# Performance work log

Measured on AMD Instinct MI355X. Metric: run time of the kernel, lower is better.

## Reference

```python
import jax, jax.numpy as jnp
import numpy as np

B, N, D, V, Y = 4, 4096, 512, 50257, 16000

def setup_inputs() -> dict:
    key = jax.random.key(0)
    ks = jax.random.split(key, 5)
    # token ids in [1, V): avoid pad_id=0 so no attention row is fully -inf
    M_s = jax.random.randint(ks[0], (B, N), 1, V)
    E_v = jax.random.normal(ks[1], (V, D), jnp.float32) * 0.02
    E_y = jax.random.normal(ks[2], (Y, D), jnp.float32) * 0.02
    s = 1.0 / np.sqrt(D)  # kaiming_uniform(a=sqrt(5)) bound for [D,D]
    W_A = jax.random.uniform(ks[3], (D, D), jnp.float32, minval=-s, maxval=s)
    W_O = jax.random.uniform(ks[4], (D, D), jnp.float32, minval=-s, maxval=s)
    gamma = jnp.ones((D,), jnp.float32)
    beta = jnp.zeros((D,), jnp.float32)
    return {"M_s": M_s, "E_v": E_v, "E_y": E_y, "W_A": W_A, "W_O": W_O,
            "gamma": gamma, "beta": beta}

def _layer_norm(x, g, b, eps=1e-5):
    mu = jnp.mean(x, axis=-1, keepdims=True)
    var = jnp.mean(jnp.square(x - mu), axis=-1, keepdims=True)
    return (x - mu) * jax.lax.rsqrt(var + eps) * g + b

def reference(M_s, E_v, E_y, W_A, W_O, gamma, beta):
    # Self-attention branch (v_q=None), dropout in eval mode (identity).
    X = E_v[M_s]                                   # [B, N, D]
    mask = (M_s != 0)                              # [B, N] padding mask
    # logits = (X @ W_A) @ X^T
    logits = jnp.einsum('bnd,de,bme->bnm', X, W_A, X)   # [B, N, N]
    logits = jnp.where(mask[:, None, :], logits, -jnp.inf)
    # positional + causal bias: D = -|i-j| with future (i<j) set to -inf
    i = jnp.arange(N, dtype=jnp.float32)[:, None]
    j = jnp.arange(N, dtype=jnp.float32)[None, :]
    dist = i - j
    bias = jnp.where(dist >= 0, -dist, -jnp.inf)        # [N, N]
    A = jax.nn.softmax(logits + bias, axis=-1)          # [B, N, N]
    Q_c = jnp.einsum('bnm,bmd,de->bne', A, X, W_O)      # [B, N, D]
    H = _layer_norm(Q_c + X, gamma, beta)               # [B, N, D]
    y_logits = jnp.einsum('bnd,yd->bny', H, E_y)        # [B, N, Y]
    return y_logits, A
```

## Files before the change

### kernel.cpp

```cpp
#include <hip/hip_runtime.h>


#define DEVINL __device__ __forceinline__

typedef __attribute__((ext_vector_type(8))) short bf16x8;
typedef __attribute__((ext_vector_type(4))) float f32x4;
typedef unsigned short u16;

#define BB 4
#define NN 4096
#define DD 512
#define YY 16000
#define YPAD 16128
#define ROWS (BB * NN)

DEVINL u16 f2bf(float x) {
  unsigned u = __float_as_uint(x);
  return (u16)((u + 0x7fffu + ((u >> 16) & 1u)) >> 16);
}

DEVINL void gload16(const void* g, void* l) {
  __builtin_amdgcn_global_load_lds(
      (const __attribute__((address_space(1))) void*)g,
      (__attribute__((address_space(3))) void*)l, 16, 0, 0);
}

DEVINL void zero_acc(f32x4 acc[4][4]) {
#pragma unroll
  for (int m = 0; m < 4; ++m)
#pragma unroll
    for (int n = 0; n < 4; ++n) {
      acc[m][n][0] = 0.f; acc[m][n][1] = 0.f;
      acc[m][n][2] = 0.f; acc[m][n][3] = 0.f;
    }
}

DEVINL void gemm_bt_core(const u16* __restrict__ A, int lda,
                         const u16* __restrict__ Bm, int ldb, int ksteps,
                         u16* sA, u16* sB, f32x4 acc[4][4], int tid) {
  const int lane = tid & 63, w = tid >> 6;
  const int wr = (w >> 1) * 64, wc = (w & 1) * 64;
  const int c0 = w * 128 + lane, c1 = c0 + 64;
  const u16* gA0 = A + (size_t)(c0 >> 2) * lda + (c0 & 3) * 8;
  const u16* gA1 = A + (size_t)(c1 >> 2) * lda + (c1 & 3) * 8;
  const u16* gB0 = Bm + (size_t)(c0 >> 2) * ldb + (c0 & 3) * 8;
  const u16* gB1 = Bm + (size_t)(c1 >> 2) * ldb + (c1 & 3) * 8;
  u16* lA0 = sA + w * 1024;  u16* lA1 = lA0 + 512;
  u16* lB0 = sB + w * 1024;  u16* lB1 = lB0 + 512;
  const int fr = lane & 15, fk = (lane >> 4) * 8;

  for (int kt = 0; kt < ksteps; ++kt) {
    __syncthreads();
    gload16(gA0 + kt * 32, lA0);
    gload16(gA1 + kt * 32, lA1);
    gload16(gB0 + kt * 32, lB0);
    gload16(gB1 + kt * 32, lB1);
    __syncthreads();
    bf16x8 af[4], bfv[4];
#pragma unroll
    for (int m = 0; m < 4; ++m)
      af[m] = *(const bf16x8*)(sA + (wr + m * 16 + fr) * 32 + fk);
#pragma unroll
    for (int n = 0; n < 4; ++n)
      bfv[n] = *(const bf16x8*)(sB + (wc + n * 16 + fr) * 32 + fk);
#pragma unroll
    for (int m = 0; m < 4; ++m)
#pragma unroll
      for (int n = 0; n < 4; ++n)
        acc[m][n] = __builtin_amdgcn_mfma_f32_16x16x32_bf16(af[m], bfv[n],
                                                            acc[m][n], 0, 0, 0);
  }
}

__global__ __launch_bounds__(128) void prep_gather(const int* __restrict__ Ms,
                                                   const float* __restrict__ Ev,
                                                   u16* __restrict__ Xb) {
  int row = blockIdx.x, tid = threadIdx.x;
  int tok = Ms[row];
  float4 v = *(const float4*)(Ev + (size_t)tok * DD + tid * 4);
  *(ushort4*)(Xb + (size_t)row * DD + tid * 4) =
      make_ushort4(f2bf(v.x), f2bf(v.y), f2bf(v.z), f2bf(v.w));
}

__global__ __launch_bounds__(256) void prep_wt(const float* __restrict__ W,
                                               u16* __restrict__ Wt) {
  int idx = blockIdx.x * 256 + threadIdx.x;
  int d = idx >> 9, e = idx & 511;
  Wt[(size_t)e * DD + d] = f2bf(W[idx]);
}

__global__ __launch_bounds__(256) void prep_ey(const float* __restrict__ Ey,
                                               u16* __restrict__ Eyb) {
  size_t i4 = (size_t)blockIdx.x * 256 + threadIdx.x;
  size_t row = i4 >> 7;
  ushort4 h;
  if (row < YY) {
    float4 v = *(const float4*)(Ey + i4 * 4);
    h = make_ushort4(f2bf(v.x), f2bf(v.y), f2bf(v.z), f2bf(v.w));
  } else {
    h = make_ushort4(0, 0, 0, 0);
  }
  *(ushort4*)(Eyb + i4 * 4) = h;
}

__global__ __launch_bounds__(256) void prep_xt(const u16* __restrict__ Xb,
                                               u16* __restrict__ XbT) {
  __shared__ u16 t[64][65];
  int tid = threadIdx.x;
  int nt = blockIdx.x, dt = blockIdx.y, b = blockIdx.z;
  const u16* src = Xb + ((size_t)b * NN + nt * 64) * DD + dt * 64;
#pragma unroll
  for (int p = 0; p < 16; ++p) {
    int e = tid + 256 * p; int r = e >> 6, c = e & 63;
    t[r][c] = src[(size_t)r * DD + c];
  }
  __syncthreads();
  u16* dst = XbT + ((size_t)b * DD + dt * 64) * NN + nt * 64;
#pragma unroll
  for (int p = 0; p < 16; ++p) {
    int e = tid + 256 * p; int r = e >> 6, c = e & 63;
    dst[(size_t)r * NN + c] = t[c][r];
  }
}

__global__ __launch_bounds__(256) void k2_xw(const u16* __restrict__ Xb,
                                             const u16* __restrict__ WAt,
                                             u16* __restrict__ XWb) {
  __shared__ u16 sA[4096], sB[4096];
  f32x4 acc[4][4]; zero_acc(acc);
  int tid = threadIdx.x;
  size_t row0 = (size_t)blockIdx.x * 128, col0 = (size_t)blockIdx.y * 128;
  gemm_bt_core(Xb + row0 * DD, DD, WAt + col0 * DD, DD, DD / 32, sA, sB, acc, tid);
  int lane = tid & 63, w = tid >> 6;
  int wr = (w >> 1) * 64, wc = (w & 1) * 64;
  int cr = (lane >> 4) * 4, cc = lane & 15;
#pragma unroll
  for (int m = 0; m < 4; ++m)
#pragma unroll
    for (int n = 0; n < 4; ++n)
#pragma unroll
      for (int r = 0; r < 4; ++r) {
        size_t gi = row0 + wr + m * 16 + cr + r;
        size_t gj = col0 + wc + n * 16 + cc;
        XWb[gi * DD + gj] = f2bf(acc[m][n][r]);
      }
}

__global__ __launch_bounds__(256) void k3_scores(const u16* __restrict__ XWb,
                                                 const u16* __restrict__ Xb,
                                                 const int* __restrict__ Ms,
                                                 float* __restrict__ Aout) {
  int ib = blockIdx.x, jb = blockIdx.y, b = blockIdx.z;
  if (jb > ib) return;
  __shared__ u16 sA[4096], sB[4096];
  f32x4 acc[4][4]; zero_acc(acc);
  int tid = threadIdx.x;
  const u16* Ap = XWb + ((size_t)b * NN + ib * 128) * DD;
  const u16* Bp = Xb  + ((size_t)b * NN + jb * 128) * DD;
  gemm_bt_core(Ap, DD, Bp, DD, DD / 32, sA, sB, acc, tid);
  int lane = tid & 63, w = tid >> 6;
  int wr = (w >> 1) * 64, wc = (w & 1) * 64;
  int cr = (lane >> 4) * 4, cc = lane & 15;
  float* Ab = Aout + (size_t)b * NN * NN;
#pragma unroll
  for (int m = 0; m < 4; ++m)
#pragma unroll
    for (int n = 0; n < 4; ++n)
#pragma unroll
      for (int r = 0; r < 4; ++r) {
        int i = ib * 128 + wr + m * 16 + cr + r;
        int j = jb * 128 + wc + n * 16 + cc;
        float v = acc[m][n][r] - (float)(i - j);
        if (j > i) v = -1e30f;
        if (Ms[b * NN + j] == 0) v = -1e30f;
        Ab[(size_t)i * NN + j] = v;
      }
}

__global__ __launch_bounds__(256) void k4_softmax(float* __restrict__ Aout,
                                                  u16* __restrict__ Abf) {
  __shared__ float srow[NN];
  __shared__ float red[4];
  size_t row = blockIdx.x;
  int i = (int)(row & (NN - 1));
  float* S = Aout + row * (size_t)NN;
  int len = i + 1, tid = threadIdx.x;
  int nv = len >> 2;
  for (int v = tid; v < nv; v += 256)
    *(float4*)(srow + v * 4) = *(const float4*)(S + v * 4);
  for (int k = (nv << 2) + tid; k < len; k += 256) srow[k] = S[k];
  __syncthreads();
  float m = -3.0e38f;
  for (int k = tid; k < len; k += 256) m = fmaxf(m, srow[k]);
#pragma unroll
  for (int o = 32; o; o >>= 1) m = fmaxf(m, __shfl_xor(m, o));
  if ((tid & 63) == 0) red[tid >> 6] = m;
  __syncthreads();
  m = fmaxf(fmaxf(red[0], red[1]), fmaxf(red[2], red[3]));
  float l = 0.f;
  for (int k = tid; k < len; k += 256) {
    float e = expf(srow[k] - m);
    srow[k] = e; l += e;
  }
  __syncthreads();
#pragma unroll
  for (int o = 32; o; o >>= 1) l += __shfl_xor(l, o);
  if ((tid & 63) == 0) red[tid >> 6] = l;
  __syncthreads();
  float inv = 1.f / (red[0] + red[1] + red[2] + red[3]);
  int padend = (len + 127) & ~127;
  u16* Ab16 = Abf + row * (size_t)NN;
  for (int k = tid; k < NN; k += 256) {
    float a = (k < len) ? srow[k] * inv : 0.f;
    S[k] = a;
    if (k < padend) Ab16[k] = f2bf(a);
  }
}

__global__ __launch_bounds__(256) void k5_ax(const u16* __restrict__ Abf,
                                             const u16* __restrict__ XbT,
                                             u16* __restrict__ AXb) {
  int ib = blockIdx.x, db = blockIdx.y, b = blockIdx.z;
  __shared__ u16 sA[4096], sB[4096];
  f32x4 acc[4][4]; zero_acc(acc);
  int tid = threadIdx.x;
  const u16* Ap = Abf + ((size_t)b * NN + ib * 128) * NN;
  const u16* Bp = XbT + ((size_t)b * DD + db * 128) * NN;
  gemm_bt_core(Ap, NN, Bp, NN, (ib + 1) * 4, sA, sB, acc, tid);
  int lane = tid & 63, w = tid >> 6;
  int wr = (w >> 1) * 64, wc = (w & 1) * 64;
  int cr = (lane >> 4) * 4, cc = lane & 15;
#pragma unroll
  for (int m = 0; m < 4; ++m)
#pragma unroll
    for (int n = 0; n < 4; ++n)
#pragma unroll
      for (int r = 0; r < 4; ++r) {
        int i = ib * 128 + wr + m * 16 + cr + r;
        int d = db * 128 + wc + n * 16 + cc;
        AXb[((size_t)b * NN + i) * DD + d] = f2bf(acc[m][n][r]);
      }
}

__global__ __launch_bounds__(256) void k6_qc(const u16* __restrict__ AXb,
                                             const u16* __restrict__ WOt,
                                             float* __restrict__ Qc32) {
  __shared__ u16 sA[4096], sB[4096];
  f32x4 acc[4][4]; zero_acc(acc);
  int tid = threadIdx.x;
  size_t row0 = (size_t)blockIdx.x * 128, col0 = (size_t)blockIdx.y * 128;
  gemm_bt_core(AXb + row0 * DD, DD, WOt + col0 * DD, DD, DD / 32, sA, sB, acc, tid);
  int lane = tid & 63, w = tid >> 6;
  int wr = (w >> 1) * 64, wc = (w & 1) * 64;
  int cr = (lane >> 4) * 4, cc = lane & 15;
#pragma unroll
  for (int m = 0; m < 4; ++m)
#pragma unroll
    for (int n = 0; n < 4; ++n)
#pragma unroll
      for (int r = 0; r < 4; ++r) {
        size_t gi = row0 + wr + m * 16 + cr + r;
        size_t gj = col0 + wc + n * 16 + cc;
        Qc32[gi * DD + gj] = acc[m][n][r];
      }
}

__global__ __launch_bounds__(128) void k6b_ln(const float* __restrict__ Qc,
                                              const float* __restrict__ Ev,
                                              const int* __restrict__ Ms,
                                              const float* __restrict__ gamma,
                                              const float* __restrict__ beta,
                                              u16* __restrict__ Hb) {
  int row = blockIdx.x, tid = threadIdx.x;
  int tok = Ms[row];
  float4 q = *(const float4*)(Qc + (size_t)row * DD + tid * 4);
  float4 x = *(const float4*)(Ev + (size_t)tok * DD + tid * 4);
  float v0 = q.x + x.x, v1 = q.y + x.y, v2 = q.z + x.z, v3 = q.w + x.w;
  float s = v0 + v1 + v2 + v3;
  float s2 = v0 * v0 + v1 * v1 + v2 * v2 + v3 * v3;
#pragma unroll
  for (int o = 32; o; o >>= 1) { s += __shfl_xor(s, o); s2 += __shfl_xor(s2, o); }
  __shared__ float r1[2], r2[2];
  int lane = tid & 63, w = tid >> 6;
  if (lane == 0) { r1[w] = s; r2[w] = s2; }
  __syncthreads();
  s = r1[0] + r1[1]; s2 = r2[0] + r2[1];
  float mu = s * (1.f / 512.f);
  float var = s2 * (1.f / 512.f) - mu * mu;
  float rs = 1.f / sqrtf(var + 1e-5f);
  float4 g  = *(const float4*)(gamma + tid * 4);
  float4 be = *(const float4*)(beta + tid * 4);
  ushort4 h = make_ushort4(f2bf((v0 - mu) * rs * g.x + be.x),
                           f2bf((v1 - mu) * rs * g.y + be.y),
                           f2bf((v2 - mu) * rs * g.z + be.z),
                           f2bf((v3 - mu) * rs * g.w + be.w));
  *(ushort4*)(Hb + (size_t)row * DD + tid * 4) = h;
}

#define K7_STAGE(kt, buf)                                      \
  {                                                            \
    const u16* a0 = Ag + (kt) * 64;                            \
    const u16* b0 = Bg + (kt) * 64;                            \
    u16* Lb = lds + (buf) * 32768;                             \
    gload16(a0 + offE0, Lb + d0);                              \
    gload16(a0 + offE1, Lb + d1);                              \
    gload16(a0 + 65536 + offE0, Lb + 8192 + d0);               \
    gload16(a0 + 65536 + offE1, Lb + 8192 + d1);               \
    gload16(b0 + offE0, Lb + 16384 + d0);                      \
    gload16(b0 + offE1, Lb + 16384 + d1);                      \
    gload16(b0 + 65536 + offE0, Lb + 24576 + d0);              \
    gload16(b0 + 65536 + offE1, Lb + 24576 + d1);              \
  }

__global__ __launch_bounds__(512, 2) void k7_logits(const u16* __restrict__ Hb,
                                                    const u16* __restrict__ Eyb,
                                                    float* __restrict__ Yout) {
  __shared__ u16 lds[65536];
  const int tid = threadIdx.x;
  const int lane = tid & 63, w = tid >> 6;
  const int wm = w >> 2, wn = w & 3;

  int id = blockIdx.x;
  int swz = (id & 7) * (4032 / 8) + (id >> 3);
  size_t row0 = (size_t)(swz & 63) * 256;
  size_t col0 = (size_t)(swz >> 6) * 256;
  const u16* Ag = Hb + row0 * DD;
  const u16* Bg = Eyb + col0 * DD;

  int offE0, offE1;
  {
    int q = tid;
    int r = (((q >> 6) >> 1) << 4) | ((q >> 2) & 15);
    int c = (((q >> 6) & 1) << 5) |
            (((q & 3) << 3) ^ (((q >> 5) & 1) << 4) ^ (((q >> 4) & 1) << 3));
    offE0 = r * DD + c;
    q = 512 + tid;
    r = (((q >> 6) >> 1) << 4) | ((q >> 2) & 15);
    c = (((q >> 6) & 1) << 5) |
        (((q & 3) << 3) ^ (((q >> 5) & 1) << 4) ^ (((q >> 4) & 1) << 3));
    offE1 = r * DD + c;
  }
  const int d0 = w * 512, d1 = 4096 + w * 512;

  int x = (lane & 15) * 64 + ((lane >> 4) & 3) * 16;
  int fxu = (x ^ (((x >> 9) & 1) << 5) ^ (((x >> 8) & 1) << 4)) >> 1;

  f32x4 acc[8][4];
#pragma unroll
  for (int m = 0; m < 8; ++m)
#pragma unroll
    for (int n = 0; n < 4; ++n) {
      acc[m][n][0] = 0.f; acc[m][n][1] = 0.f;
      acc[m][n][2] = 0.f; acc[m][n][3] = 0.f;
    }

  K7_STAGE(0, 0);
  K7_STAGE(1, 1);
  asm volatile("s_waitcnt vmcnt(8)" ::: "memory");
  __syncthreads();

  for (int c = 0; c < 8; ++c) {
    const u16* L = lds + (c & 1) * 32768;
    const u16* pa = L + wm * 8192;
    const u16* pb = L + 16384 + (wn >> 1) * 8192 + (wn & 1) * 4096;
    bf16x8 af[4][2], bf[4][2];
#pragma unroll
    for (int n = 0; n < 2; ++n)
#pragma unroll
      for (int ks = 0; ks < 2; ++ks)
        bf[n][ks] = *(const bf16x8*)(pb + (n * 2 + ks) * 512 + fxu);
#pragma unroll
    for (int m = 0; m < 4; ++m)
#pragma unroll
      for (int ks = 0; ks < 2; ++ks)
        af[m][ks] = *(const bf16x8*)(pa + (m * 2 + ks) * 512 + fxu);
    __builtin_amdgcn_s_setprio(1);
#pragma unroll
    for (int m = 0; m < 4; ++m)
#pragma unroll
      for (int n = 0; n < 2; ++n)
#pragma unroll
        for (int ks = 0; ks < 2; ++ks)
          acc[m][n] = __builtin_amdgcn_mfma_f32_16x16x32_bf16(
              af[m][ks], bf[n][ks], acc[m][n], 0, 0, 0);
    __builtin_amdgcn_s_setprio(0);
#pragma unroll
    for (int n = 2; n < 4; ++n)
#pragma unroll
      for (int ks = 0; ks < 2; ++ks)
        bf[n][ks] = *(const bf16x8*)(pb + (n * 2 + ks) * 512 + fxu);
    __builtin_amdgcn_s_setprio(1);
#pragma unroll
    for (int m = 0; m < 4; ++m)
#pragma unroll
      for (int n = 2; n < 4; ++n)
#pragma unroll
        for (int ks = 0; ks < 2; ++ks)
          acc[m][n] = __builtin_amdgcn_mfma_f32_16x16x32_bf16(
              af[m][ks], bf[n][ks], acc[m][n], 0, 0, 0);
    __builtin_amdgcn_s_setprio(0);
#pragma unroll
    for (int m = 0; m < 4; ++m)
#pragma unroll
      for (int ks = 0; ks < 2; ++ks)
        af[m][ks] = *(const bf16x8*)(pa + ((m + 4) * 2 + ks) * 512 + fxu);
    __builtin_amdgcn_s_setprio(1);
#pragma unroll
    for (int m = 0; m < 4; ++m)
#pragma unroll
      for (int n = 0; n < 2; ++n)
#pragma unroll
        for (int ks = 0; ks < 2; ++ks)
          acc[m + 4][n] = __builtin_amdgcn_mfma_f32_16x16x32_bf16(
              af[m][ks], bf[n][ks], acc[m + 4][n], 0, 0, 0);
#pragma unroll
    for (int m = 0; m < 4; ++m)
#pragma unroll
      for (int n = 2; n < 4; ++n)
#pragma unroll
        for (int ks = 0; ks < 2; ++ks)
          acc[m + 4][n] = __builtin_amdgcn_mfma_f32_16x16x32_bf16(
              af[m][ks], bf[n][ks], acc[m + 4][n], 0, 0, 0);
    __builtin_amdgcn_s_setprio(0);

    __syncthreads();
    if (c < 6) {
      K7_STAGE(c + 2, c & 1);
      asm volatile("s_waitcnt vmcnt(8)" ::: "memory");
    } else if (c == 6) {
      asm volatile("s_waitcnt vmcnt(0)" ::: "memory");
    }
    __syncthreads();
  }

  const int cr = (lane >> 4) * 4, cc = lane & 15;
#pragma unroll
  for (int m = 0; m < 8; ++m)
#pragma unroll
    for (int n = 0; n < 4; ++n) {
      size_t gj = col0 + wn * 64 + n * 16 + cc;
      if (gj < YY) {
        size_t gi = row0 + wm * 128 + m * 16 + cr;
#pragma unroll
        for (int rr = 0; rr < 4; ++rr)
          Yout[(gi + rr) * (size_t)YY + gj] = acc[m][n][rr];
      }
    }
}

extern "C" void kernel_launch(void* const* d_in, const int* in_sizes, int n_in,
                              void* d_out, int out_size, void* d_ws, size_t ws_size,
                              hipStream_t stream) {
  (void)in_sizes; (void)n_in; (void)out_size; (void)ws_size;
  const int*   Ms    = (const int*)d_in[0];
  const float* Ev    = (const float*)d_in[1];
  const float* Ey    = (const float*)d_in[2];
  const float* WA    = (const float*)d_in[3];
  const float* WO    = (const float*)d_in[4];
  const float* gamma = (const float*)d_in[5];
  const float* beta  = (const float*)d_in[6];

  float* Yout = (float*)d_out;
  float* Aout = Yout + (size_t)BB * NN * YY;

  char* w = (char*)d_ws;
  u16* Xb  = (u16*)w; w += (size_t)ROWS * DD * 2;
  u16* XbT = (u16*)w; w += (size_t)BB * DD * NN * 2;
  u16* XWb = (u16*)w; w += (size_t)ROWS * DD * 2;
  u16* AXb = (u16*)w; w += (size_t)ROWS * DD * 2;
  u16* Hb  = (u16*)w; w += (size_t)ROWS * DD * 2;
  u16* WAt = (u16*)w; w += (size_t)DD * DD * 2;
  u16* WOt = (u16*)w; w += (size_t)DD * DD * 2;
  u16* Eyb = (u16*)w; w += (size_t)YPAD * DD * 2;
  u16* Abf = (u16*)w; w += (size_t)ROWS * NN * 2;
  float* Qc32 = (float*)XbT;

  prep_gather<<<ROWS, 128, 0, stream>>>(Ms, Ev, Xb);
  prep_wt<<<1024, 256, 0, stream>>>(WA, WAt);
  prep_wt<<<1024, 256, 0, stream>>>(WO, WOt);
  prep_ey<<<YPAD * DD / 4 / 256, 256, 0, stream>>>(Ey, Eyb);
  prep_xt<<<dim3(NN / 64, DD / 64, BB), 256, 0, stream>>>(Xb, XbT);
  k2_xw<<<dim3(ROWS / 128, DD / 128), 256, 0, stream>>>(Xb, WAt, XWb);
  k3_scores<<<dim3(NN / 128, NN / 128, BB), 256, 0, stream>>>(XWb, Xb, Ms, Aout);
  k4_softmax<<<ROWS, 256, 0, stream>>>(Aout, Abf);
  k5_ax<<<dim3(NN / 128, DD / 128, BB), 256, 0, stream>>>(Abf, XbT, AXb);
  k6_qc<<<dim3(ROWS / 128, DD / 128), 256, 0, stream>>>(AXb, WOt, Qc32);
  k6b_ln<<<ROWS, 128, 0, stream>>>(Qc32, Ev, Ms, gamma, beta, Hb);
  k7_logits<<<dim3(64 * 63), 512, 0, stream>>>(Hb, Eyb, Yout);
}
```

Baseline: 936.4 us.

## Compact triangular grids, vectorize softmax, tile weight transpose, reuse bf16 X in LN

The score kernel now launches only lower-triangular tiles, decoding the tile index with a sqrt, instead of launching the full square grid and exiting early. The AX kernel reorders its blocks so long and short causal rows are interleaved for better load balance. Softmax now reads, reduces and writes with float4 and ushort4 accesses and uses fast __expf. The weight transpose goes through an LDS tile so global accesses are coalesced. LayerNorm reads the bf16 gathered X instead of re-gathering fp32 embeddings, which saves a gather but adds bf16 rounding to the residual path.

After: 895.4 us. 4.4% less time.

```diff
diff --git a/kernel.cpp b/kernel.cpp
--- a/kernel.cpp
+++ b/kernel.cpp
@@ -18,6 +18,8 @@
   unsigned u = __float_as_uint(x);
   return (u16)((u + 0x7fffu + ((u >> 16) & 1u)) >> 16);
 }
+
+DEVINL float bf2f(u16 h) { return __uint_as_float((unsigned)h << 16); }
 
 DEVINL void gload16(const void* g, void* l) {
   __builtin_amdgcn_global_load_lds(
@@ -84,9 +86,19 @@
 
 __global__ __launch_bounds__(256) void prep_wt(const float* __restrict__ W,
                                                u16* __restrict__ Wt) {
-  int idx = blockIdx.x * 256 + threadIdx.x;
-  int d = idx >> 9, e = idx & 511;
-  Wt[(size_t)e * DD + d] = f2bf(W[idx]);
+  __shared__ u16 t[64][65];
+  int dt = blockIdx.x, et = blockIdx.y, tid = threadIdx.x;
+#pragma unroll
+  for (int p = 0; p < 16; ++p) {
+    int e = tid + 256 * p; int r = e >> 6, c = e & 63;
+    t[r][c] = f2bf(W[(size_t)(dt * 64 + r) * DD + et * 64 + c]);
+  }
+  __syncthreads();
+#pragma unroll
+  for (int p = 0; p < 16; ++p) {
+    int e = tid + 256 * p; int r = e >> 6, c = e & 63;
+    Wt[(size_t)(et * 64 + r) * DD + dt * 64 + c] = t[c][r];
+  }
 }
 
 __global__ __launch_bounds__(256) void prep_ey(const float* __restrict__ Ey,
@@ -150,8 +162,11 @@
                                                  const u16* __restrict__ Xb,
                                                  const int* __restrict__ Ms,
                                                  float* __restrict__ Aout) {
-  int ib = blockIdx.x, jb = blockIdx.y, b = blockIdx.z;
-  if (jb > ib) return;
+  int t = blockIdx.x, b = blockIdx.z;
+  int ib = (int)((sqrtf(8.f * (float)t + 1.f) - 1.f) * 0.5f);
+  while ((ib + 1) * (ib + 2) / 2 <= t) ++ib;
+  while (ib * (ib + 1) / 2 > t) --ib;
+  int jb = t - ib * (ib + 1) / 2;
   __shared__ u16 sA[4096], sB[4096];
   f32x4 acc[4][4]; zero_acc(acc);
   int tid = threadIdx.x;
@@ -185,42 +200,59 @@
   int i = (int)(row & (NN - 1));
   float* S = Aout + row * (size_t)NN;
   int len = i + 1, tid = threadIdx.x;
-  int nv = len >> 2;
-  for (int v = tid; v < nv; v += 256)
+  int lenp = (len + 3) & ~3;
+  int nc = lenp >> 2;
+  int padend = (len + 127) & ~127;
+  for (int v = tid; v < nc; v += 256)
     *(float4*)(srow + v * 4) = *(const float4*)(S + v * 4);
-  for (int k = (nv << 2) + tid; k < len; k += 256) srow[k] = S[k];
   __syncthreads();
   float m = -3.0e38f;
-  for (int k = tid; k < len; k += 256) m = fmaxf(m, srow[k]);
+  for (int v = tid; v < nc; v += 256) {
+    float4 x = *(const float4*)(srow + v * 4);
+    m = fmaxf(m, fmaxf(fmaxf(x.x, x.y), fmaxf(x.z, x.w)));
+  }
 #pragma unroll
   for (int o = 32; o; o >>= 1) m = fmaxf(m, __shfl_xor(m, o));
   if ((tid & 63) == 0) red[tid >> 6] = m;
   __syncthreads();
   m = fmaxf(fmaxf(red[0], red[1]), fmaxf(red[2], red[3]));
+  __syncthreads();
   float l = 0.f;
-  for (int k = tid; k < len; k += 256) {
-    float e = expf(srow[k] - m);
-    srow[k] = e; l += e;
-  }
-  __syncthreads();
+  for (int v = tid; v < nc; v += 256) {
+    float4 x = *(const float4*)(srow + v * 4);
+    x.x = __expf(x.x - m); x.y = __expf(x.y - m);
+    x.z = __expf(x.z - m); x.w = __expf(x.w - m);
+    l += (x.x + x.y) + (x.z + x.w);
+    *(float4*)(srow + v * 4) = x;
+  }
 #pragma unroll
   for (int o = 32; o; o >>= 1) l += __shfl_xor(l, o);
   if ((tid & 63) == 0) red[tid >> 6] = l;
   __syncthreads();
   float inv = 1.f / (red[0] + red[1] + red[2] + red[3]);
-  int padend = (len + 127) & ~127;
   u16* Ab16 = Abf + row * (size_t)NN;
-  for (int k = tid; k < NN; k += 256) {
-    float a = (k < len) ? srow[k] * inv : 0.f;
-    S[k] = a;
-    if (k < padend) Ab16[k] = f2bf(a);
+  for (int v = tid; v < NN / 4; v += 256) {
+    int k = v * 4;
+    float4 a = make_float4(0.f, 0.f, 0.f, 0.f);
+    if (k < lenp) {
+      float4 x = *(const float4*)(srow + k);
+      a = make_float4(x.x * inv, x.y * inv, x.z * inv, x.w * inv);
+    }
+    *(float4*)(S + k) = a;
+    if (k < padend)
+      *(ushort4*)(Ab16 + k) =
+          make_ushort4(f2bf(a.x), f2bf(a.y), f2bf(a.z), f2bf(a.w));
   }
 }
 
 __global__ __launch_bounds__(256) void k5_ax(const u16* __restrict__ Abf,
                                              const u16* __restrict__ XbT,
                                              u16* __restrict__ AXb) {
-  int ib = blockIdx.x, db = blockIdx.y, b = blockIdx.z;
+  int u = blockIdx.x;
+  int half = u >> 8, v = u & 255;
+  int ib = v & 31; if (half) ib = 31 - ib;
+  int db = (v >> 5) & 3;
+  int b = (half << 1) | (v >> 7);
   __shared__ u16 sA[4096], sB[4096];
   f32x4 acc[4][4]; zero_acc(acc);
   int tid = threadIdx.x;
@@ -266,16 +298,15 @@
 }
 
 __global__ __launch_bounds__(128) void k6b_ln(const float* __restrict__ Qc,
-                                              const float* __restrict__ Ev,
-                                              const int* __restrict__ Ms,
+                                              const u16* __restrict__ Xb,
                                               const float* __restrict__ gamma,
                                               const float* __restrict__ beta,
                                               u16* __restrict__ Hb) {
   int row = blockIdx.x, tid = threadIdx.x;
-  int tok = Ms[row];
   float4 q = *(const float4*)(Qc + (size_t)row * DD + tid * 4);
-  float4 x = *(const float4*)(Ev + (size_t)tok * DD + tid * 4);
-  float v0 = q.x + x.x, v1 = q.y + x.y, v2 = q.z + x.z, v3 = q.w + x.w;
+  ushort4 xu = *(const ushort4*)(Xb + (size_t)row * DD + tid * 4);
+  float v0 = q.x + bf2f(xu.x), v1 = q.y + bf2f(xu.y);
+  float v2 = q.z + bf2f(xu.z), v3 = q.w + bf2f(xu.w);
   float s = v0 + v1 + v2 + v3;
   float s2 = v0 * v0 + v1 * v1 + v2 * v2 + v3 * v3;
 #pragma unroll
@@ -476,15 +507,15 @@
   float* Qc32 = (float*)XbT;
 
   prep_gather<<<ROWS, 128, 0, stream>>>(Ms, Ev, Xb);
-  prep_wt<<<1024, 256, 0, stream>>>(WA, WAt);
-  prep_wt<<<1024, 256, 0, stream>>>(WO, WOt);
+  prep_wt<<<dim3(8, 8), 256, 0, stream>>>(WA, WAt);
+  prep_wt<<<dim3(8, 8), 256, 0, stream>>>(WO, WOt);
   prep_ey<<<YPAD * DD / 4 / 256, 256, 0, stream>>>(Ey, Eyb);
   prep_xt<<<dim3(NN / 64, DD / 64, BB), 256, 0, stream>>>(Xb, XbT);
   k2_xw<<<dim3(ROWS / 128, DD / 128), 256, 0, stream>>>(Xb, WAt, XWb);
-  k3_scores<<<dim3(NN / 128, NN / 128, BB), 256, 0, stream>>>(XWb, Xb, Ms, Aout);
+  k3_scores<<<dim3(528, 1, BB), 256, 0, stream>>>(XWb, Xb, Ms, Aout);
   k4_softmax<<<ROWS, 256, 0, stream>>>(Aout, Abf);
-  k5_ax<<<dim3(NN / 128, DD / 128, BB), 256, 0, stream>>>(Abf, XbT, AXb);
+  k5_ax<<<512, 256, 0, stream>>>(Abf, XbT, AXb);
   k6_qc<<<dim3(ROWS / 128, DD / 128), 256, 0, stream>>>(AXb, WOt, Qc32);
-  k6b_ln<<<ROWS, 128, 0, stream>>>(Qc32, Ev, Ms, gamma, beta, Hb);
+  k6b_ln<<<ROWS, 128, 0, stream>>>(Qc32, Xb, gamma, beta, Hb);
   k7_logits<<<dim3(64 * 63), 512, 0, stream>>>(Hb, Eyb, Yout);
 }
```
